# Optimization experiments

Measured on AMD Instinct MI355X. Metric: run time of the kernel, lower is better.

## Reference

```python
import jax, jax.numpy as jnp
import numpy as np


def setup_inputs() -> dict:
    key = jax.random.key(0)
    k1, k2, k3, k4 = jax.random.split(key, 4)
    B, S, K, R, DIN, DOUT = 8, 2048, 16, 16, 2048, 2048
    h = jax.random.normal(k1, (B, S, DIN), dtype=jnp.float32)
    alpha = jax.random.uniform(k2, (B, K), dtype=jnp.float32)
    A_bank = jax.random.normal(k3, (K, R, DIN), dtype=jnp.float32) * (1.0 / np.sqrt(DIN))
    B_bank = jax.random.normal(k4, (K, DOUT, R), dtype=jnp.float32) * (1.0 / np.sqrt(R))
    return {"h": h, "alpha": alpha, "A_bank": A_bank, "B_bank": B_bank}


def reference(h, alpha, A_bank, B_bank):
    # Mix K low-rank bases per sample, then apply low-rank delta to h.
    A_mixed = jnp.einsum('bk,kri->bri', alpha, A_bank)   # [B, r, d_in]
    B_mixed = jnp.einsum('bk,kor->bor', alpha, B_bank)   # [B, d_out, r]
    z = jnp.einsum('bri,bsi->bsr', A_mixed, h)           # [B, S, r]
    delta = jnp.einsum('bor,bsr->bso', B_mixed, z)       # [B, S, d_out]
    return delta
```

## Files before the change

### kernel.cpp

```cpp
#include <hip/hip_runtime.h>

typedef unsigned int u32;
typedef float f32x4 __attribute__((ext_vector_type(4)));

#define BB 8
#define SS 2048
#define KK 16
#define RR 16
#define DIN 2048
#define DOUT 2048

__global__ void __launch_bounds__(256) mix_kernel(
    const float* __restrict__ alpha,
    const float* __restrict__ A_bank,
    const float* __restrict__ B_bank,
    float* __restrict__ Am,
    float* __restrict__ Bm)
{
    int t = blockIdx.x * 256 + threadIdx.x;
    const int half = BB * RR * DIN;
    if (t < half) {
        int i = t & (DIN - 1);
        int r = (t >> 11) & (RR - 1);
        int b = t >> 15;
        float acc = 0.f;
#pragma unroll
        for (int k = 0; k < KK; ++k)
            acc += alpha[b * KK + k] * A_bank[(k * RR + r) * DIN + i];
        Am[t] = acc;
    } else {
        int u = t - half;
        int r = u & (RR - 1);
        int o = (u >> 4) & (DOUT - 1);
        int b = u >> 15;
        float acc = 0.f;
#pragma unroll
        for (int k = 0; k < KK; ++k)
            acc += alpha[b * KK + k] * B_bank[(k * DOUT + o) * RR + r];
        Bm[u] = acc;
    }
}

__global__ void __launch_bounds__(256, 3) z_kernel(
    const float* __restrict__ h,
    const float* __restrict__ Am,
    float* __restrict__ z)
{
    int b = blockIdx.y;
    int wid = threadIdx.x >> 6;
    int lane = threadIdx.x & 63;
    int s0 = blockIdx.x * 16 + wid * 4;
    const float* hb = h + (size_t)b * SS * DIN + (size_t)s0 * DIN;
    const float* Ab = Am + (size_t)b * RR * DIN;

    float a[64];
#pragma unroll
    for (int v = 0; v < 64; ++v) a[v] = 0.f;

#pragma unroll 1
    for (int t = 0; t < 8; ++t) {
        int i0 = t * 256 + lane * 4;
        float4 hv0 = *(const float4*)(hb + i0);
        float4 hv1 = *(const float4*)(hb + DIN + i0);
        float4 hv2 = *(const float4*)(hb + 2 * DIN + i0);
        float4 hv3 = *(const float4*)(hb + 3 * DIN + i0);
#pragma unroll
        for (int r = 0; r < 16; ++r) {
            float4 av = *(const float4*)(Ab + r * DIN + i0);
            a[0 * 16 + r] += hv0.x * av.x + hv0.y * av.y + hv0.z * av.z + hv0.w * av.w;
            a[1 * 16 + r] += hv1.x * av.x + hv1.y * av.y + hv1.z * av.z + hv1.w * av.w;
            a[2 * 16 + r] += hv2.x * av.x + hv2.y * av.y + hv2.z * av.z + hv2.w * av.w;
            a[3 * 16 + r] += hv3.x * av.x + hv3.y * av.y + hv3.z * av.z + hv3.w * av.w;
        }
    }

#pragma unroll
    for (int off = 32; off >= 1; off >>= 1) {
        bool up = (lane & off) != 0;
#pragma unroll
        for (int v = 0; v < off; ++v) {
            float send = up ? a[v] : a[v + off];
            float keep = up ? a[v + off] : a[v];
            a[v] = keep + __shfl_xor(send, off, 64);
        }
    }
    z[(size_t)(b * SS + s0) * RR + lane] = a[0];
}

__global__ void __launch_bounds__(256, 4) delta_kernel(
    const float* __restrict__ z,
    const float* __restrict__ Bm,
    float* __restrict__ out)
{
    int b = blockIdx.z;
    int s0 = blockIdx.y * 64;
    int o0 = blockIdx.x * 1024 + threadIdx.x * 4;

    const float* wp = Bm + ((size_t)b * DOUT + o0) * RR;
    float w[4][16];
#pragma unroll
    for (int j = 0; j < 4; ++j) {
#pragma unroll
        for (int q = 0; q < 4; ++q) {
            float4 p = *(const float4*)(wp + j * 16 + q * 4);
            w[j][q * 4 + 0] = p.x; w[j][q * 4 + 1] = p.y;
            w[j][q * 4 + 2] = p.z; w[j][q * 4 + 3] = p.w;
        }
    }

    const float* zp = z + (size_t)(b * SS + s0) * RR;
    float* op = out + ((size_t)b * SS + s0) * DOUT + o0;

#pragma unroll 2
    for (int s = 0; s < 64; ++s) {
        float4 z0 = *(const float4*)(zp + s * 16);
        float4 z1 = *(const float4*)(zp + s * 16 + 4);
        float4 z2 = *(const float4*)(zp + s * 16 + 8);
        float4 z3 = *(const float4*)(zp + s * 16 + 12);
        float zz[16] = {z0.x, z0.y, z0.z, z0.w, z1.x, z1.y, z1.z, z1.w,
                        z2.x, z2.y, z2.z, z2.w, z3.x, z3.y, z3.z, z3.w};
        float rj[4];
#pragma unroll
        for (int j = 0; j < 4; ++j) {
            float acc = 0.f;
#pragma unroll
            for (int r = 0; r < 16; ++r) acc += w[j][r] * zz[r];
            rj[j] = acc;
        }
        f32x4 res;
        res.x = rj[0]; res.y = rj[1]; res.z = rj[2]; res.w = rj[3];
        __builtin_nontemporal_store(res, (f32x4*)(op + (size_t)s * DOUT));
    }
}

extern "C" void kernel_launch(void* const* d_in, const int* in_sizes, int n_in,
                              void* d_out, int out_size, void* d_ws, size_t ws_size,
                              hipStream_t stream)
{
    const float* h      = (const float*)d_in[0];
    const float* alpha  = (const float*)d_in[1];
    const float* A_bank = (const float*)d_in[2];
    const float* B_bank = (const float*)d_in[3];
    float* out = (float*)d_out;

    float* Am = (float*)d_ws;
    float* Bm = Am + BB * RR * DIN;
    float* z  = Bm + BB * DOUT * RR;

    mix_kernel<<<2048, 256, 0, stream>>>(alpha, A_bank, B_bank, Am, Bm);
    z_kernel<<<dim3(128, 8), 256, 0, stream>>>(h, Am, z);
    delta_kernel<<<dim3(2, 32, 8), 256, 0, stream>>>(z, Bm, out);
}
```

Measured before the change: 262.3 us.

## Fuse z projection and delta expansion into one kernel via shared memory

After: 259.6 us. No clear change (-1.0%).

```diff
diff --git a/kernel.cpp b/kernel.cpp
--- a/kernel.cpp
+++ b/kernel.cpp
@@ -41,16 +41,21 @@
     }
 }
 
-__global__ void __launch_bounds__(256, 3) z_kernel(
+__global__ void __launch_bounds__(256, 3) fused_kernel(
     const float* __restrict__ h,
     const float* __restrict__ Am,
-    float* __restrict__ z)
+    const float* __restrict__ Bm,
+    float* __restrict__ out)
 {
+    __shared__ float zt[16 * 16];
+
     int b = blockIdx.y;
     int wid = threadIdx.x >> 6;
     int lane = threadIdx.x & 63;
-    int s0 = blockIdx.x * 16 + wid * 4;
-    const float* hb = h + (size_t)b * SS * DIN + (size_t)s0 * DIN;
+    int s0 = blockIdx.x * 16;
+    int sw = s0 + wid * 4;
+
+    const float* hb = h + (size_t)b * SS * DIN + (size_t)sw * DIN;
     const float* Ab = Am + (size_t)b * RR * DIN;
 
     float a[64];
@@ -60,13 +65,13 @@
 #pragma unroll 1
     for (int t = 0; t < 8; ++t) {
         int i0 = t * 256 + lane * 4;
-        float4 hv0 = *(const float4*)(hb + i0);
-        float4 hv1 = *(const float4*)(hb + DIN + i0);
-        float4 hv2 = *(const float4*)(hb + 2 * DIN + i0);
-        float4 hv3 = *(const float4*)(hb + 3 * DIN + i0);
+        f32x4 hv0 = __builtin_nontemporal_load((const f32x4*)(hb + i0));
+        f32x4 hv1 = __builtin_nontemporal_load((const f32x4*)(hb + DIN + i0));
+        f32x4 hv2 = __builtin_nontemporal_load((const f32x4*)(hb + 2 * DIN + i0));
+        f32x4 hv3 = __builtin_nontemporal_load((const f32x4*)(hb + 3 * DIN + i0));
 #pragma unroll
         for (int r = 0; r < 16; ++r) {
-            float4 av = *(const float4*)(Ab + r * DIN + i0);
+            f32x4 av = *(const f32x4*)(Ab + r * DIN + i0);
             a[0 * 16 + r] += hv0.x * av.x + hv0.y * av.y + hv0.z * av.z + hv0.w * av.w;
             a[1 * 16 + r] += hv1.x * av.x + hv1.y * av.y + hv1.z * av.z + hv1.w * av.w;
             a[2 * 16 + r] += hv2.x * av.x + hv2.y * av.y + hv2.z * av.z + hv2.w * av.w;
@@ -84,52 +89,46 @@
             a[v] = keep + __shfl_xor(send, off, 64);
         }
     }
-    z[(size_t)(b * SS + s0) * RR + lane] = a[0];
-}
+    zt[wid * 64 + lane] = a[0];
+    __syncthreads();
 
-__global__ void __launch_bounds__(256, 4) delta_kernel(
-    const float* __restrict__ z,
-    const float* __restrict__ Bm,
-    float* __restrict__ out)
-{
-    int b = blockIdx.z;
-    int s0 = blockIdx.y * 64;
-    int o0 = blockIdx.x * 1024 + threadIdx.x * 4;
+    float* op = out + ((size_t)b * SS + s0) * DOUT;
 
-    const float* wp = Bm + ((size_t)b * DOUT + o0) * RR;
-    float w[4][16];
-#pragma unroll
-    for (int j = 0; j < 4; ++j) {
-#pragma unroll
-        for (int q = 0; q < 4; ++q) {
-            float4 p = *(const float4*)(wp + j * 16 + q * 4);
-            w[j][q * 4 + 0] = p.x; w[j][q * 4 + 1] = p.y;
-            w[j][q * 4 + 2] = p.z; w[j][q * 4 + 3] = p.w;
-        }
-    }
-
-    const float* zp = z + (size_t)(b * SS + s0) * RR;
-    float* op = out + ((size_t)b * SS + s0) * DOUT + o0;
-
-#pragma unroll 2
-    for (int s = 0; s < 64; ++s) {
-        float4 z0 = *(const float4*)(zp + s * 16);
-        float4 z1 = *(const float4*)(zp + s * 16 + 4);
-        float4 z2 = *(const float4*)(zp + s * 16 + 8);
-        float4 z3 = *(const float4*)(zp + s * 16 + 12);
-        float zz[16] = {z0.x, z0.y, z0.z, z0.w, z1.x, z1.y, z1.z, z1.w,
-                        z2.x, z2.y, z2.z, z2.w, z3.x, z3.y, z3.z, z3.w};
-        float rj[4];
+#pragma unroll 1
+    for (int oc = 0; oc < 2; ++oc) {
+        int o0 = oc * 1024 + threadIdx.x * 4;
+        const float* wp = Bm + ((size_t)b * DOUT + o0) * RR;
+        float w[4][16];
 #pragma unroll
         for (int j = 0; j < 4; ++j) {
-            float acc = 0.f;
 #pragma unroll
-            for (int r = 0; r < 16; ++r) acc += w[j][r] * zz[r];
-            rj[j] = acc;
+            for (int q = 0; q < 4; ++q) {
+                f32x4 p = *(const f32x4*)(wp + j * RR + q * 4);
+                w[j][q * 4 + 0] = p.x; w[j][q * 4 + 1] = p.y;
+                w[j][q * 4 + 2] = p.z; w[j][q * 4 + 3] = p.w;
+            }
         }
-        f32x4 res;
-        res.x = rj[0]; res.y = rj[1]; res.z = rj[2]; res.w = rj[3];
-        __builtin_nontemporal_store(res, (f32x4*)(op + (size_t)s * DOUT));
+#pragma unroll 4
+        for (int s = 0; s < 16; ++s) {
+            float zz[16];
+#pragma unroll
+            for (int q = 0; q < 4; ++q) {
+                f32x4 zv = *(const f32x4*)(zt + s * 16 + q * 4);
+                zz[q * 4 + 0] = zv.x; zz[q * 4 + 1] = zv.y;
+                zz[q * 4 + 2] = zv.z; zz[q * 4 + 3] = zv.w;
+            }
+            float rj[4];
+#pragma unroll
+            for (int j = 0; j < 4; ++j) {
+                float acc = 0.f;
+#pragma unroll
+                for (int r = 0; r < 16; ++r) acc += w[j][r] * zz[r];
+                rj[j] = acc;
+            }
+            f32x4 res;
+            res.x = rj[0]; res.y = rj[1]; res.z = rj[2]; res.w = rj[3];
+            __builtin_nontemporal_store(res, (f32x4*)(op + (size_t)s * DOUT + o0));
+        }
     }
 }
 
@@ -145,9 +144,7 @@
 
     float* Am = (float*)d_ws;
     float* Bm = Am + BB * RR * DIN;
-    float* z  = Bm + BB * DOUT * RR;
 
     mix_kernel<<<2048, 256, 0, stream>>>(alpha, A_bank, B_bank, Am, Bm);
-    z_kernel<<<dim3(128, 8), 256, 0, stream>>>(h, Am, z);
-    delta_kernel<<<dim3(2, 32, 8), 256, 0, stream>>>(z, Bm, out);
+    fused_kernel<<<dim3(128, 8), 256, 0, stream>>>(h, Am, Bm, out);
 }
```
